# Performance work log

Measured on AMD Instinct MI355X. Metric: run time of the kernel, lower is better.

## Reference

```python
import jax, jax.numpy as jnp
import numpy as np

B = 48        # graphs per batch
NODES = 330   # hardcoded in forward (x.view(batch_size, 330, hidden))
N = B * NODES # 15840 nodes
DEG = 16
E = N * DEG   # 253440 edges
IN_CH = 128
HID = 256
OUT_CH = 1
EDGE_DIM = 5
EPS = 1e-5


def _lin(key, out_f, in_f):
    k1, k2 = jax.random.split(key)
    s = 1.0 / np.sqrt(in_f)
    W = jax.random.uniform(k1, (out_f, in_f), minval=-s, maxval=s, dtype=jnp.float32)
    b = jax.random.uniform(k2, (out_f,), minval=-s, maxval=s, dtype=jnp.float32)
    return W, b


def setup_inputs() -> dict:
    key = jax.random.key(0)
    ks = jax.random.split(key, 10)
    x = jax.random.normal(ks[0], (N, IN_CH), dtype=jnp.float32)
    edge_index = jax.random.randint(ks[1], (2, E), 0, N, dtype=jnp.int32)
    edge_attr = jax.random.normal(ks[2], (E, EDGE_DIM), dtype=jnp.float32)
    batch = (jnp.arange(N, dtype=jnp.int32) // NODES)
    Wq, bq = _lin(ks[3], HID, IN_CH)
    Wk, bk = _lin(ks[4], HID, IN_CH)
    Wv, bv = _lin(ks[5], HID, IN_CH)
    se = 1.0 / np.sqrt(EDGE_DIM)
    We = jax.random.uniform(ks[6], (HID, EDGE_DIM), minval=-se, maxval=se, dtype=jnp.float32)  # lin_edge, bias=False
    Wskip, bskip = _lin(ks[7], HID, IN_CH)
    ln_g = jnp.ones((IN_CH,), jnp.float32); ln_b = jnp.zeros((IN_CH,), jnp.float32)
    bn_g = jnp.ones((HID,), jnp.float32); bn_b = jnp.zeros((HID,), jnp.float32)
    W1, b1 = _lin(ks[8], HID, HID)
    Wr, br = _lin(ks[9], OUT_CH, HID)
    return dict(x=x, edge_index=edge_index, edge_attr=edge_attr, batch=batch,
                Wq=Wq, bq=bq, Wk=Wk, bk=bk, Wv=Wv, bv=bv, We=We,
                Wskip=Wskip, bskip=bskip, ln_g=ln_g, ln_b=ln_b,
                bn_g=bn_g, bn_b=bn_b, W1=W1, b1=b1, Wr=Wr, br=br)


def _forward(x, edge_index, edge_attr, batch,
             Wq, bq, Wk, bk, Wv, bv, We, Wskip, bskip,
             ln_g, ln_b, bn_g, bn_b, W1, b1, Wr, br):
    n = x.shape[0]
    bs = batch.shape[0] // NODES
    # self.norm -> assumed LayerNorm over features
    mu = x.mean(-1, keepdims=True)
    var = x.var(-1, keepdims=True)
    x = (x - mu) / jnp.sqrt(var + EPS) * ln_g + ln_b

    # TransformerConv (heads=1, edge_dim=5, root_weight=True)
    src, dst = edge_index[0], edge_index[1]
    q = x @ Wq.T + bq                      # [N, HID]
    k = x @ Wk.T + bk
    v = x @ Wv.T + bv
    e = edge_attr @ We.T                   # [E, HID]
    ke = k[src] + e                        # edge-conditioned keys
    ve = v[src] + e                        # edge-conditioned values
    alpha = (q[dst] * ke).sum(-1) / jnp.sqrt(jnp.float32(HID))  # [E]
    m = jax.ops.segment_max(alpha, dst, num_segments=n)
    a = jnp.exp(alpha - m[dst])
    z = jax.ops.segment_sum(a, dst, num_segments=n)
    a = a / (z[dst] + 1e-16)               # PyG softmax guard
    out = jax.ops.segment_sum(a[:, None] * ve, dst, num_segments=n)
    out = out + x @ Wskip.T + bskip        # root/skip connection

    # BatchNorm1d (training-mode batch stats) + relu
    bm = out.mean(0)
    bv_ = out.var(0)
    out = (out - bm) / jnp.sqrt(bv_ + EPS) * bn_g + bn_b
    out = jax.nn.relu(out)

    # pooling chain over the node axis: 330 -> 110 -> 36 -> 18
    h = out.reshape(bs, NODES, HID).transpose(0, 2, 1)   # [B, HID, 330]
    h = h.reshape(bs, HID, 110, 3).max(-1)               # k3 s3
    h = h[:, :, :108].reshape(bs, HID, 36, 3).max(-1)    # k3 s3 (floor)
    h = h.reshape(bs, HID, 18, 2).max(-1)                # k2 s2
    h = h.transpose(0, 2, 1)                             # [B, 18, HID]

    h = jax.nn.relu(h @ W1.T + b1)
    c = (h @ Wr.T + br).mean(axis=1)                     # [B, OUT]
    return jax.nn.sigmoid(c).squeeze(-1)                 # [B]


def reference(x, edge_index, edge_attr, batch, Wq, bq, Wk, bk, Wv, bv, We,
              Wskip, bskip, ln_g, ln_b, bn_g, bn_b, W1, b1, Wr, br):
    return _forward(x, edge_index, edge_attr, batch, Wq, bq, Wk, bk, Wv, bv,
                    We, Wskip, bskip, ln_g, ln_b, bn_g, bn_b, W1, b1, Wr, br)
```

## Files before the change

kernel.cpp:

```cpp
#include <hip/hip_runtime.h>
#include <math.h>

#define NNODES 15840
#define NEDGES 253440
#define INCH 128
#define HIDC 256
#define BGR 48
#define GNODES 330

__device__ inline unsigned short f2bf(float f) {
  union { float f; unsigned int u; } v; v.f = f;
  unsigned int u = v.u;
  u += 0x7fff + ((u >> 16) & 1);
  return (unsigned short)(u >> 16);
}
__device__ inline float bf2f(unsigned short h) {
  union { unsigned int u; float f; } v; v.u = ((unsigned int)h) << 16;
  return v.f;
}

__global__ void ln_kernel(const float* __restrict__ x, const float* __restrict__ g,
                          const float* __restrict__ b, float* __restrict__ xln) {
  int wid = (blockIdx.x * blockDim.x + threadIdx.x) >> 6;
  int lane = threadIdx.x & 63;
  if (wid >= NNODES) return;
  float2 v = *(const float2*)(x + (size_t)wid * INCH + lane * 2);
  float s = v.x + v.y;
#pragma unroll
  for (int o = 32; o > 0; o >>= 1) s += __shfl_xor(s, o);
  float mean = s * (1.0f / INCH);
  float d0 = v.x - mean, d1 = v.y - mean;
  float sq = d0 * d0 + d1 * d1;
#pragma unroll
  for (int o = 32; o > 0; o >>= 1) sq += __shfl_xor(sq, o);
  float rstd = rsqrtf(sq * (1.0f / INCH) + 1e-5f);
  float2 gg = *(const float2*)(g + lane * 2);
  float2 bb = *(const float2*)(b + lane * 2);
  float2 o2;
  o2.x = d0 * rstd * gg.x + bb.x;
  o2.y = d1 * rstd * gg.y + bb.y;
  *(float2*)(xln + (size_t)wid * INCH + lane * 2) = o2;
}

#define GBM 128
#define GBN 128
#define GBK 32
#define KD 128
__global__ __launch_bounds__(256) void gemm_qkvs(
    const float* __restrict__ xln,
    const float* __restrict__ Wq, const float* __restrict__ bq,
    const float* __restrict__ Wk, const float* __restrict__ bk,
    const float* __restrict__ Wv, const float* __restrict__ bv,
    const float* __restrict__ Ws, const float* __restrict__ bs,
    float* __restrict__ QS, unsigned short* __restrict__ KV) {
  __shared__ float As[GBK][GBM];
  __shared__ float Bs[GBK][GBN];
  int t = threadIdx.x;
  int m0 = blockIdx.x * GBM;
  int jb = blockIdx.y;
  int mat = jb >> 1;
  const float* W; const float* bias;
  switch (mat) {
    case 0:  W = Wq; bias = bq; break;
    case 1:  W = Wk; bias = bk; break;
    case 2:  W = Wv; bias = bv; break;
    default: W = Ws; bias = bs; break;
  }
  int j0 = (jb & 1) * GBN;

  int r = t & 127;
  int half = t >> 7;
  int tx = t & 15, ty = t >> 4;

  int gr = m0 + r;
  bool okA = gr < NNODES;
  const float* arow = xln + (size_t)gr * KD;
  const float* brow = W + (size_t)(j0 + r) * KD;

  float acc[8][8] = {};

  for (int k0 = 0; k0 < KD; k0 += GBK) {
#pragma unroll
    for (int i = 0; i < 4; i++) {
      int lk = half * 16 + i * 4;
      int kc = k0 + lk;
      float4 av = okA ? *(const float4*)(arow + kc) : make_float4(0.f, 0.f, 0.f, 0.f);
      As[lk + 0][r] = av.x; As[lk + 1][r] = av.y;
      As[lk + 2][r] = av.z; As[lk + 3][r] = av.w;
      float4 bvv = *(const float4*)(brow + kc);
      Bs[lk + 0][r] = bvv.x; Bs[lk + 1][r] = bvv.y;
      Bs[lk + 2][r] = bvv.z; Bs[lk + 3][r] = bvv.w;
    }
    __syncthreads();
#pragma unroll 2
    for (int k = 0; k < GBK; k++) {
      float4 a0 = *(const float4*)&As[k][ty * 4];
      float4 a1 = *(const float4*)&As[k][64 + ty * 4];
      float4 b0 = *(const float4*)&Bs[k][tx * 4];
      float4 b1 = *(const float4*)&Bs[k][64 + tx * 4];
      float aa[8] = {a0.x, a0.y, a0.z, a0.w, a1.x, a1.y, a1.z, a1.w};
      float bb[8] = {b0.x, b0.y, b0.z, b0.w, b1.x, b1.y, b1.z, b1.w};
#pragma unroll
      for (int ar = 0; ar < 8; ar++)
#pragma unroll
        for (int ac = 0; ac < 8; ac++) acc[ar][ac] += aa[ar] * bb[ac];
    }
    __syncthreads();
  }

  float4 bb0 = *(const float4*)(bias + j0 + tx * 4);
  float4 bb1 = *(const float4*)(bias + j0 + 64 + tx * 4);
  int sec = (mat == 0 || mat == 1) ? 0 : 256;
  bool isF32 = (mat == 0 || mat == 3);
  int col0 = sec + j0 + tx * 4;
#pragma unroll
  for (int ar = 0; ar < 8; ar++) {
    int grow = m0 + ((ar < 4) ? (ty * 4 + ar) : (64 + ty * 4 + ar - 4));
    if (grow < NNODES) {
      float4 o0, o1;
      o0.x = acc[ar][0] + bb0.x; o0.y = acc[ar][1] + bb0.y;
      o0.z = acc[ar][2] + bb0.z; o0.w = acc[ar][3] + bb0.w;
      o1.x = acc[ar][4] + bb1.x; o1.y = acc[ar][5] + bb1.y;
      o1.z = acc[ar][6] + bb1.z; o1.w = acc[ar][7] + bb1.w;
      if (isF32) {
        *(float4*)(QS + (size_t)grow * 512 + col0) = o0;
        *(float4*)(QS + (size_t)grow * 512 + col0 + 64) = o1;
      } else {
        ushort4 h0, h1;
        h0.x = f2bf(o0.x); h0.y = f2bf(o0.y); h0.z = f2bf(o0.z); h0.w = f2bf(o0.w);
        h1.x = f2bf(o1.x); h1.y = f2bf(o1.y); h1.z = f2bf(o1.z); h1.w = f2bf(o1.w);
        *(ushort4*)(KV + (size_t)grow * 512 + col0) = h0;
        *(ushort4*)(KV + (size_t)grow * 512 + col0 + 64) = h1;
      }
    }
  }
}

__global__ void count_kernel(const int* __restrict__ dst, int* __restrict__ deg) {
  int e = blockIdx.x * blockDim.x + threadIdx.x;
  if (e < NEDGES) atomicAdd(&deg[dst[e]], 1);
}

__global__ void scan_kernel(const int* __restrict__ deg, int* __restrict__ row_start) {
  __shared__ int wsum[16];
  __shared__ int carry_s;
  int t = threadIdx.x;
  int lane = t & 63, w = t >> 6;
  if (t == 0) carry_s = 0;
  __syncthreads();
  for (int base = 0; base < NNODES; base += 1024) {
    int i = base + t;
    int v = (i < NNODES) ? deg[i] : 0;
    int inc = v;
#pragma unroll
    for (int o = 1; o < 64; o <<= 1) {
      int nv = __shfl_up(inc, o);
      if (lane >= o) inc += nv;
    }
    if (lane == 63) wsum[w] = inc;
    __syncthreads();
    if (w == 0 && lane < 16) {
      int ws = wsum[lane];
#pragma unroll
      for (int o = 1; o < 16; o <<= 1) {
        int nv = __shfl_up(ws, o);
        if (lane >= o) ws += nv;
      }
      wsum[lane] = ws;
    }
    __syncthreads();
    int wexcl = (w > 0) ? wsum[w - 1] : 0;
    int chunk_total = wsum[15];
    int cl = carry_s;
    if (i < NNODES) row_start[i] = cl + wexcl + inc - v;
    __syncthreads();
    if (t == 0) carry_s += chunk_total;
  }
  __syncthreads();
  if (t == 0) row_start[NNODES] = carry_s;
}

__global__ void scatter_kernel(const int* __restrict__ src, const int* __restrict__ dst,
                               const int* __restrict__ row_start, int* __restrict__ cursor,
                               const float* __restrict__ ea, int* __restrict__ src_perm,
                               float* __restrict__ ea_perm) {
  int e = blockIdx.x * blockDim.x + threadIdx.x;
  if (e < NEDGES) {
    int d = dst[e];
    int pos = row_start[d] + atomicAdd(&cursor[d], 1);
    src_perm[pos] = src[e];
    const float* ap = ea + (size_t)e * 5;
    float* op = ea_perm + (size_t)pos * 5;
#pragma unroll
    for (int i = 0; i < 5; i++) op[i] = ap[i];
  }
}

__global__ __launch_bounds__(256) void agg_kernel(
    const float* __restrict__ QS, const unsigned short* __restrict__ KV,
    const float* __restrict__ ea_perm, const float* __restrict__ We,
    const int* __restrict__ src_perm, const int* __restrict__ row_start,
    float* __restrict__ outb) {
  int t = threadIdx.x;
  int nd = blockIdx.x * 4 + (t >> 6);
  int lane = t & 63;
  if (nd >= NNODES) return;

  float4 q = *(const float4*)(QS + (size_t)nd * 512 + 4 * lane);

  float c5[5];
  {
    float wp0[5], wp1[5], wp2[5], wp3[5];
#pragma unroll
    for (int d = 0; d < 5; d++) {
      wp0[d] = We[(4 * lane + 0) * 5 + d];
      wp1[d] = We[(4 * lane + 1) * 5 + d];
      wp2[d] = We[(4 * lane + 2) * 5 + d];
      wp3[d] = We[(4 * lane + 3) * 5 + d];
    }
#pragma unroll
    for (int d = 0; d < 5; d++) {
      float s = q.x * wp0[d] + q.y * wp1[d] + q.z * wp2[d] + q.w * wp3[d];
#pragma unroll
      for (int o = 32; o > 0; o >>= 1) s += __shfl_xor(s, o);
      c5[d] = s;
    }
  }

  int beg = row_start[nd], end = row_start[nd + 1];
  float m = -INFINITY, z = 0.0f;
  float ax = 0.f, ay = 0.f, az = 0.f, aw = 0.f;
  float ea_acc[5] = {0.f, 0.f, 0.f, 0.f, 0.f};

  int j = beg;
  for (; j + 4 <= end; j += 4) {
    int s0 = src_perm[j], s1 = src_perm[j + 1], s2 = src_perm[j + 2], s3 = src_perm[j + 3];
    const unsigned short* b0 = KV + (size_t)s0 * 512 + 4 * lane;
    const unsigned short* b1 = KV + (size_t)s1 * 512 + 4 * lane;
    const unsigned short* b2 = KV + (size_t)s2 * 512 + 4 * lane;
    const unsigned short* b3 = KV + (size_t)s3 * 512 + 4 * lane;
    ushort4 hk0 = *(const ushort4*)b0;
    ushort4 hk1 = *(const ushort4*)b1;
    ushort4 hk2 = *(const ushort4*)b2;
    ushort4 hk3 = *(const ushort4*)b3;
    ushort4 hv0 = *(const ushort4*)(b0 + 256);
    ushort4 hv1 = *(const ushort4*)(b1 + 256);
    ushort4 hv2 = *(const ushort4*)(b2 + 256);
    ushort4 hv3 = *(const ushort4*)(b3 + 256);
    float eat[4][5];
    {
      const float* ap = ea_perm + (size_t)j * 5;
#pragma unroll
      for (int i = 0; i < 4; i++)
#pragma unroll
        for (int d = 0; d < 5; d++) eat[i][d] = ap[i * 5 + d];
    }
    float p0 = q.x * bf2f(hk0.x) + q.y * bf2f(hk0.y) + q.z * bf2f(hk0.z) + q.w * bf2f(hk0.w);
    float p1 = q.x * bf2f(hk1.x) + q.y * bf2f(hk1.y) + q.z * bf2f(hk1.z) + q.w * bf2f(hk1.w);
    float p2 = q.x * bf2f(hk2.x) + q.y * bf2f(hk2.y) + q.z * bf2f(hk2.z) + q.w * bf2f(hk2.w);
    float p3 = q.x * bf2f(hk3.x) + q.y * bf2f(hk3.y) + q.z * bf2f(hk3.z) + q.w * bf2f(hk3.w);
#pragma unroll
    for (int o = 32; o > 0; o >>= 1) {
      p0 += __shfl_xor(p0, o); p1 += __shfl_xor(p1, o);
      p2 += __shfl_xor(p2, o); p3 += __shfl_xor(p3, o);
    }
    float dt0 = 0.f, dt1 = 0.f, dt2 = 0.f, dt3 = 0.f;
#pragma unroll
    for (int d = 0; d < 5; d++) {
      dt0 += c5[d] * eat[0][d]; dt1 += c5[d] * eat[1][d];
      dt2 += c5[d] * eat[2][d]; dt3 += c5[d] * eat[3][d];
    }
    float al0 = (p0 + dt0) * 0.0625f, al1 = (p1 + dt1) * 0.0625f;
    float al2 = (p2 + dt2) * 0.0625f, al3 = (p3 + dt3) * 0.0625f;
    float bm = fmaxf(fmaxf(al0, al1), fmaxf(al2, al3));
    float nm = fmaxf(m, bm);
    float sc = __expf(m - nm);
    float w0 = __expf(al0 - nm), w1 = __expf(al1 - nm);
    float w2 = __expf(al2 - nm), w3 = __expf(al3 - nm);
    z = z * sc + (w0 + w1 + w2 + w3);
    ax = ax * sc + w0 * bf2f(hv0.x) + w1 * bf2f(hv1.x) + w2 * bf2f(hv2.x) + w3 * bf2f(hv3.x);
    ay = ay * sc + w0 * bf2f(hv0.y) + w1 * bf2f(hv1.y) + w2 * bf2f(hv2.y) + w3 * bf2f(hv3.y);
    az = az * sc + w0 * bf2f(hv0.z) + w1 * bf2f(hv1.z) + w2 * bf2f(hv2.z) + w3 * bf2f(hv3.z);
    aw = aw * sc + w0 * bf2f(hv0.w) + w1 * bf2f(hv1.w) + w2 * bf2f(hv2.w) + w3 * bf2f(hv3.w);
#pragma unroll
    for (int d = 0; d < 5; d++)
      ea_acc[d] = ea_acc[d] * sc + w0 * eat[0][d] + w1 * eat[1][d] + w2 * eat[2][d] + w3 * eat[3][d];
    m = nm;
  }
  for (; j < end; j++) {
    int s = src_perm[j];
    const unsigned short* bp = KV + (size_t)s * 512 + 4 * lane;
    ushort4 hk = *(const ushort4*)bp;
    ushort4 hv = *(const ushort4*)(bp + 256);
    float eat[5];
    const float* ap = ea_perm + (size_t)j * 5;
#pragma unroll
    for (int d = 0; d < 5; d++) eat[d] = ap[d];
    float p = q.x * bf2f(hk.x) + q.y * bf2f(hk.y) + q.z * bf2f(hk.z) + q.w * bf2f(hk.w);
#pragma unroll
    for (int o = 32; o > 0; o >>= 1) p += __shfl_xor(p, o);
    float dt = 0.f;
#pragma unroll
    for (int d = 0; d < 5; d++) dt += c5[d] * eat[d];
    float al = (p + dt) * 0.0625f;
    float nm = fmaxf(m, al);
    float sc = __expf(m - nm);
    float w = __expf(al - nm);
    z = z * sc + w;
    ax = ax * sc + w * bf2f(hv.x); ay = ay * sc + w * bf2f(hv.y);
    az = az * sc + w * bf2f(hv.z); aw = aw * sc + w * bf2f(hv.w);
#pragma unroll
    for (int d = 0; d < 5; d++) ea_acc[d] = ea_acc[d] * sc + w * eat[d];
    m = nm;
  }

  float inv = 1.0f / (z + 1e-16f);
  float4 sk = *(const float4*)(QS + (size_t)nd * 512 + 256 + 4 * lane);
  float efx = 0.f, efy = 0.f, efz = 0.f, efw = 0.f;
#pragma unroll
  for (int d = 0; d < 5; d++) {
    float ead = ea_acc[d];
    efx += We[(4 * lane + 0) * 5 + d] * ead;
    efy += We[(4 * lane + 1) * 5 + d] * ead;
    efz += We[(4 * lane + 2) * 5 + d] * ead;
    efw += We[(4 * lane + 3) * 5 + d] * ead;
  }
  float4 o;
  o.x = (ax + efx) * inv + sk.x;
  o.y = (ay + efy) * inv + sk.y;
  o.z = (az + efz) * inv + sk.z;
  o.w = (aw + efw) * inv + sk.w;
  *(float4*)(outb + (size_t)nd * HIDC + 4 * lane) = o;
}

__global__ void bnstat_kernel(const float* __restrict__ outb, float* __restrict__ sums,
                              float* __restrict__ sumsq) {
  int f = threadIdx.x;
  int r0 = blockIdx.x * 120;
  float s = 0.0f, sq = 0.0f;
  for (int r = 0; r < 120; r++) {
    float v = outb[(size_t)(r0 + r) * HIDC + f];
    s += v; sq += v * v;
  }
  atomicAdd(&sums[f], s);
  atomicAdd(&sumsq[f], sq);
}

__global__ void pool_mlp_kernel(const float* __restrict__ outb, const float* __restrict__ sums,
                                const float* __restrict__ sumsq, const float* __restrict__ bng,
                                const float* __restrict__ bnb, const float* __restrict__ W1,
                                const float* __restrict__ b1, const float* __restrict__ Wr,
                                float* __restrict__ c) {
  __shared__ float hs[HIDC];
  __shared__ float red[HIDC];
  int bt = blockIdx.x, t = threadIdx.x;
  int b = bt / 18, tt = bt % 18;
  float mean = sums[t] * (1.0f / NNODES);
  float var = sumsq[t] * (1.0f / NNODES) - mean * mean;
  float scale = bng[t] * rsqrtf(var + 1e-5f);
  float shift = bnb[t] - mean * scale;
  int base = b * GNODES + tt * 18;
  float mx = -INFINITY;
  for (int r = 0; r < 18; r++) {
    float v = outb[(size_t)(base + r) * HIDC + t];
    mx = fmaxf(mx, fmaxf(v * scale + shift, 0.0f));
  }
  hs[t] = mx;
  __syncthreads();
  const float4* hv = (const float4*)hs;
  const float4* w = (const float4*)(W1 + t * HIDC);
  float acc = b1[t];
#pragma unroll 8
  for (int i = 0; i < HIDC / 4; i++) {
    float4 xi = hv[i]; float4 ww = w[i];
    acc += xi.x * ww.x + xi.y * ww.y + xi.z * ww.z + xi.w * ww.w;
  }
  red[t] = fmaxf(acc, 0.0f) * Wr[t];
  __syncthreads();
#pragma unroll
  for (int s = 128; s > 0; s >>= 1) {
    if (t < s) red[t] += red[t + s];
    __syncthreads();
  }
  if (t == 0) atomicAdd(&c[b], red[0] * (1.0f / 18.0f));
}

__global__ void final_kernel(const float* __restrict__ c, const float* __restrict__ br,
                             float* __restrict__ out) {
  int b = threadIdx.x;
  if (b < BGR) out[b] = 1.0f / (1.0f + expf(-(c[b] + br[0])));
}

extern "C" void kernel_launch(void* const* d_in, const int* in_sizes, int n_in,
                              void* d_out, int out_size, void* d_ws, size_t ws_size,
                              hipStream_t stream) {
  const float* x   = (const float*)d_in[0];
  const int*   ei  = (const int*)d_in[1];
  const float* ea  = (const float*)d_in[2];
  const float* Wq  = (const float*)d_in[4];  const float* bq  = (const float*)d_in[5];
  const float* Wk  = (const float*)d_in[6];  const float* bk  = (const float*)d_in[7];
  const float* Wv  = (const float*)d_in[8];  const float* bv  = (const float*)d_in[9];
  const float* We  = (const float*)d_in[10];
  const float* Wsk = (const float*)d_in[11]; const float* bsk = (const float*)d_in[12];
  const float* lng = (const float*)d_in[13]; const float* lnb = (const float*)d_in[14];
  const float* bng = (const float*)d_in[15]; const float* bnb = (const float*)d_in[16];
  const float* W1  = (const float*)d_in[17]; const float* b1  = (const float*)d_in[18];
  const float* Wr  = (const float*)d_in[19]; const float* br  = (const float*)d_in[20];
  float* outp = (float*)d_out;

  const int* srcArr = ei;
  const int* dstArr = ei + NEDGES;

  char* ws = (char*)d_ws;
  size_t off = 0;
  auto alloc = [&](size_t bytes) -> void* {
    void* p = ws + off;
    off += (bytes + 255) & ~(size_t)255;
    return p;
  };
  float*          xln       = (float*)alloc((size_t)NNODES * INCH * 4);
  float*          QS        = (float*)alloc((size_t)NNODES * 512 * 4);
  unsigned short* KV        = (unsigned short*)alloc((size_t)NNODES * 512 * 2);
  float*          outb      = (float*)alloc((size_t)NNODES * HIDC * 4);
  int*            row_start = (int*)alloc((size_t)(NNODES + 1) * 4);
  int*            src_perm  = (int*)alloc((size_t)NEDGES * 4);
  float*          ea_perm   = (float*)alloc((size_t)NEDGES * 5 * 4);
  size_t zn = (size_t)NNODES * 2 + HIDC * 2 + BGR;
  int* zblock = (int*)alloc(zn * 4);
  int*   deg    = zblock;
  int*   cursor = zblock + NNODES;
  float* sums   = (float*)(zblock + 2 * NNODES);
  float* sumsq  = sums + HIDC;
  float* cacc   = sumsq + HIDC;

  hipMemsetAsync(zblock, 0, zn * 4, stream);

  ln_kernel<<<NNODES / 4, 256, 0, stream>>>(x, lng, lnb, xln);
  dim3 ggrid((NNODES + GBM - 1) / GBM, 8);
  gemm_qkvs<<<ggrid, 256, 0, stream>>>(xln, Wq, bq, Wk, bk, Wv, bv, Wsk, bsk, QS, KV);
  count_kernel<<<NEDGES / 256, 256, 0, stream>>>(dstArr, deg);
  scan_kernel<<<1, 1024, 0, stream>>>(deg, row_start);
  scatter_kernel<<<NEDGES / 256, 256, 0, stream>>>(srcArr, dstArr, row_start, cursor, ea,
                                                   src_perm, ea_perm);
  agg_kernel<<<NNODES / 4, 256, 0, stream>>>(QS, KV, ea_perm, We, src_perm, row_start, outb);
  bnstat_kernel<<<132, 256, 0, stream>>>(outb, sums, sumsq);
  pool_mlp_kernel<<<BGR * 18, 256, 0, stream>>>(outb, sums, sumsq, bng, bnb, W1, b1, Wr, cacc);
  final_kernel<<<1, 64, 0, stream>>>(cacc, br, outp);
}
```

Measured before the change: 296.7 us.

## Use split-bf16 MFMA projection GEMM and fixed-slot edge buckets in a fused prep kernel

```diff
diff --git a/kernel.cpp b/kernel.cpp
--- a/kernel.cpp
+++ b/kernel.cpp
@@ -7,6 +7,10 @@
 #define HIDC 256
 #define BGR 48
 #define GNODES 330
+#define SLOT 56
+
+typedef __attribute__((ext_vector_type(8))) short bf16x8;
+typedef __attribute__((ext_vector_type(4))) float f32x4;
 
 __device__ inline unsigned short f2bf(float f) {
   union { float f; unsigned int u; } v; v.f = f;
@@ -19,187 +23,158 @@
   return v.f;
 }
 
-__global__ void ln_kernel(const float* __restrict__ x, const float* __restrict__ g,
-                          const float* __restrict__ b, float* __restrict__ xln) {
-  int wid = (blockIdx.x * blockDim.x + threadIdx.x) >> 6;
-  int lane = threadIdx.x & 63;
-  if (wid >= NNODES) return;
-  float2 v = *(const float2*)(x + (size_t)wid * INCH + lane * 2);
-  float s = v.x + v.y;
-#pragma unroll
-  for (int o = 32; o > 0; o >>= 1) s += __shfl_xor(s, o);
-  float mean = s * (1.0f / INCH);
-  float d0 = v.x - mean, d1 = v.y - mean;
-  float sq = d0 * d0 + d1 * d1;
-#pragma unroll
-  for (int o = 32; o > 0; o >>= 1) sq += __shfl_xor(sq, o);
-  float rstd = rsqrtf(sq * (1.0f / INCH) + 1e-5f);
-  float2 gg = *(const float2*)(g + lane * 2);
-  float2 bb = *(const float2*)(b + lane * 2);
-  float2 o2;
-  o2.x = d0 * rstd * gg.x + bb.x;
-  o2.y = d1 * rstd * gg.y + bb.y;
-  *(float2*)(xln + (size_t)wid * INCH + lane * 2) = o2;
-}
-
-#define GBM 128
-#define GBN 128
-#define GBK 32
-#define KD 128
-__global__ __launch_bounds__(256) void gemm_qkvs(
-    const float* __restrict__ xln,
+#define LN_BLOCKS 3960
+#define WC_BLOCKS 128
+#define BUILD_BLOCKS 990
+__global__ __launch_bounds__(256) void prep_kernel(
+    const float* __restrict__ x, const float* __restrict__ g, const float* __restrict__ b,
+    unsigned short* __restrict__ Xhi, unsigned short* __restrict__ Xlo,
     const float* __restrict__ Wq, const float* __restrict__ bq,
     const float* __restrict__ Wk, const float* __restrict__ bk,
     const float* __restrict__ Wv, const float* __restrict__ bv,
     const float* __restrict__ Ws, const float* __restrict__ bs,
+    unsigned short* __restrict__ Whi, unsigned short* __restrict__ Wlo,
+    float* __restrict__ bbig,
+    const int* __restrict__ src, const int* __restrict__ dst,
+    const float* __restrict__ ea, int* __restrict__ cursor,
+    int* __restrict__ src_perm, float* __restrict__ ea_perm) {
+  int blk = blockIdx.x, t = threadIdx.x;
+  if (blk < LN_BLOCKS) {
+    int wid = blk * 4 + (t >> 6);
+    int lane = t & 63;
+    float2 v = *(const float2*)(x + (size_t)wid * INCH + lane * 2);
+    float s = v.x + v.y;
+#pragma unroll
+    for (int o = 32; o > 0; o >>= 1) s += __shfl_xor(s, o);
+    float mean = s * (1.0f / INCH);
+    float d0 = v.x - mean, d1 = v.y - mean;
+    float sq = d0 * d0 + d1 * d1;
+#pragma unroll
+    for (int o = 32; o > 0; o >>= 1) sq += __shfl_xor(sq, o);
+    float rstd = rsqrtf(sq * (1.0f / INCH) + 1e-5f);
+    float2 gg = *(const float2*)(g + lane * 2);
+    float2 bb = *(const float2*)(b + lane * 2);
+    float o0 = d0 * rstd * gg.x + bb.x;
+    float o1 = d1 * rstd * gg.y + bb.y;
+    unsigned short h0 = f2bf(o0), h1 = f2bf(o1);
+    unsigned short l0 = f2bf(o0 - bf2f(h0)), l1 = f2bf(o1 - bf2f(h1));
+    ushort2 hh; hh.x = h0; hh.y = h1;
+    ushort2 ll; ll.x = l0; ll.y = l1;
+    *(ushort2*)(Xhi + (size_t)wid * INCH + lane * 2) = hh;
+    *(ushort2*)(Xlo + (size_t)wid * INCH + lane * 2) = ll;
+  } else if (blk < LN_BLOCKS + WC_BLOCKS) {
+    int idx = (blk - LN_BLOCKS) * 256 + t;
+    int n = idx >> 5;
+    int k0 = (idx & 31) * 4;
+    const float* W; const float* bias;
+    switch (n >> 8) {
+      case 0:  W = Wq; bias = bq; break;
+      case 1:  W = Wk; bias = bk; break;
+      case 2:  W = Wv; bias = bv; break;
+      default: W = Ws; bias = bs; break;
+    }
+    int r = n & 255;
+    float4 w4 = *(const float4*)(W + (size_t)r * 128 + k0);
+    ushort4 hi, lo;
+    hi.x = f2bf(w4.x); lo.x = f2bf(w4.x - bf2f(hi.x));
+    hi.y = f2bf(w4.y); lo.y = f2bf(w4.y - bf2f(hi.y));
+    hi.z = f2bf(w4.z); lo.z = f2bf(w4.z - bf2f(hi.z));
+    hi.w = f2bf(w4.w); lo.w = f2bf(w4.w - bf2f(hi.w));
+    *(ushort4*)(Whi + (size_t)n * 128 + k0) = hi;
+    *(ushort4*)(Wlo + (size_t)n * 128 + k0) = lo;
+    if (idx < 1024) {
+      const float* bsrc;
+      switch (idx >> 8) {
+        case 0:  bsrc = bq; break;
+        case 1:  bsrc = bk; break;
+        case 2:  bsrc = bv; break;
+        default: bsrc = bs; break;
+      }
+      bbig[idx] = bsrc[idx & 255];
+    }
+  } else {
+    int e = (blk - LN_BLOCKS - WC_BLOCKS) * 256 + t;
+    if (e < NEDGES) {
+      int d = dst[e];
+      int pos = atomicAdd(&cursor[d], 1);
+      if (pos < SLOT) {
+        int slot = d * SLOT + pos;
+        src_perm[slot] = src[e];
+        const float* ap = ea + (size_t)e * 5;
+        float* op = ea_perm + (size_t)slot * 5;
+#pragma unroll
+        for (int i = 0; i < 5; i++) op[i] = ap[i];
+      }
+    }
+  }
+}
+
+__global__ __launch_bounds__(64) void gemm_mfma(
+    const unsigned short* __restrict__ Xhi, const unsigned short* __restrict__ Xlo,
+    const unsigned short* __restrict__ Whi, const unsigned short* __restrict__ Wlo,
+    const float* __restrict__ bbig,
     float* __restrict__ QS, unsigned short* __restrict__ KV) {
-  __shared__ float As[GBK][GBM];
-  __shared__ float Bs[GBK][GBN];
-  int t = threadIdx.x;
-  int m0 = blockIdx.x * GBM;
-  int jb = blockIdx.y;
-  int mat = jb >> 1;
-  const float* W; const float* bias;
-  switch (mat) {
-    case 0:  W = Wq; bias = bq; break;
-    case 1:  W = Wk; bias = bk; break;
-    case 2:  W = Wv; bias = bv; break;
-    default: W = Ws; bias = bs; break;
-  }
-  int j0 = (jb & 1) * GBN;
-
-  int r = t & 127;
-  int half = t >> 7;
-  int tx = t & 15, ty = t >> 4;
-
-  int gr = m0 + r;
-  bool okA = gr < NNODES;
-  const float* arow = xln + (size_t)gr * KD;
-  const float* brow = W + (size_t)(j0 + r) * KD;
-
-  float acc[8][8] = {};
-
-  for (int k0 = 0; k0 < KD; k0 += GBK) {
-#pragma unroll
-    for (int i = 0; i < 4; i++) {
-      int lk = half * 16 + i * 4;
-      int kc = k0 + lk;
-      float4 av = okA ? *(const float4*)(arow + kc) : make_float4(0.f, 0.f, 0.f, 0.f);
-      As[lk + 0][r] = av.x; As[lk + 1][r] = av.y;
-      As[lk + 2][r] = av.z; As[lk + 3][r] = av.w;
-      float4 bvv = *(const float4*)(brow + kc);
-      Bs[lk + 0][r] = bvv.x; Bs[lk + 1][r] = bvv.y;
-      Bs[lk + 2][r] = bvv.z; Bs[lk + 3][r] = bvv.w;
-    }
-    __syncthreads();
-#pragma unroll 2
-    for (int k = 0; k < GBK; k++) {
-      float4 a0 = *(const float4*)&As[k][ty * 4];
-      float4 a1 = *(const float4*)&As[k][64 + ty * 4];
-      float4 b0 = *(const float4*)&Bs[k][tx * 4];
-      float4 b1 = *(const float4*)&Bs[k][64 + tx * 4];
-      float aa[8] = {a0.x, a0.y, a0.z, a0.w, a1.x, a1.y, a1.z, a1.w};
-      float bb[8] = {b0.x, b0.y, b0.z, b0.w, b1.x, b1.y, b1.z, b1.w};
-#pragma unroll
-      for (int ar = 0; ar < 8; ar++)
-#pragma unroll
-        for (int ac = 0; ac < 8; ac++) acc[ar][ac] += aa[ar] * bb[ac];
-    }
-    __syncthreads();
-  }
-
-  float4 bb0 = *(const float4*)(bias + j0 + tx * 4);
-  float4 bb1 = *(const float4*)(bias + j0 + 64 + tx * 4);
-  int sec = (mat == 0 || mat == 1) ? 0 : 256;
-  bool isF32 = (mat == 0 || mat == 3);
-  int col0 = sec + j0 + tx * 4;
-#pragma unroll
-  for (int ar = 0; ar < 8; ar++) {
-    int grow = m0 + ((ar < 4) ? (ty * 4 + ar) : (64 + ty * 4 + ar - 4));
-    if (grow < NNODES) {
-      float4 o0, o1;
-      o0.x = acc[ar][0] + bb0.x; o0.y = acc[ar][1] + bb0.y;
-      o0.z = acc[ar][2] + bb0.z; o0.w = acc[ar][3] + bb0.w;
-      o1.x = acc[ar][4] + bb1.x; o1.y = acc[ar][5] + bb1.y;
-      o1.z = acc[ar][6] + bb1.z; o1.w = acc[ar][7] + bb1.w;
-      if (isF32) {
-        *(float4*)(QS + (size_t)grow * 512 + col0) = o0;
-        *(float4*)(QS + (size_t)grow * 512 + col0 + 64) = o1;
-      } else {
-        ushort4 h0, h1;
-        h0.x = f2bf(o0.x); h0.y = f2bf(o0.y); h0.z = f2bf(o0.z); h0.w = f2bf(o0.w);
-        h1.x = f2bf(o1.x); h1.y = f2bf(o1.y); h1.z = f2bf(o1.z); h1.w = f2bf(o1.w);
-        *(ushort4*)(KV + (size_t)grow * 512 + col0) = h0;
-        *(ushort4*)(KV + (size_t)grow * 512 + col0 + 64) = h1;
+  int lane = threadIdx.x;
+  int m0 = blockIdx.x * 32;
+  int quad = lane >> 4;
+  int lr = lane & 15;
+
+  bf16x8 A[2][2][4];
+#pragma unroll
+  for (int tI = 0; tI < 2; tI++) {
+    const unsigned short* ph = Xhi + (size_t)(m0 + tI * 16 + lr) * 128 + quad * 8;
+    const unsigned short* pl = Xlo + (size_t)(m0 + tI * 16 + lr) * 128 + quad * 8;
+#pragma unroll
+    for (int kf = 0; kf < 4; kf++) {
+      A[tI][0][kf] = *(const bf16x8*)(ph + kf * 32);
+      A[tI][1][kf] = *(const bf16x8*)(pl + kf * 32);
+    }
+  }
+
+  for (int nt = 0; nt < 64; nt++) {
+    int n0 = nt * 16;
+    const unsigned short* wh = Whi + (size_t)(n0 + lr) * 128 + quad * 8;
+    const unsigned short* wl = Wlo + (size_t)(n0 + lr) * 128 + quad * 8;
+    bf16x8 Bh[4], Bl[4];
+#pragma unroll
+    for (int kf = 0; kf < 4; kf++) {
+      Bh[kf] = *(const bf16x8*)(wh + kf * 32);
+      Bl[kf] = *(const bf16x8*)(wl + kf * 32);
+    }
+    f32x4 acc0 = {0.f, 0.f, 0.f, 0.f}, acc1 = {0.f, 0.f, 0.f, 0.f};
+#pragma unroll
+    for (int kf = 0; kf < 4; kf++) {
+      acc0 = __builtin_amdgcn_mfma_f32_16x16x32_bf16(A[0][0][kf], Bh[kf], acc0, 0, 0, 0);
+      acc1 = __builtin_amdgcn_mfma_f32_16x16x32_bf16(A[1][0][kf], Bh[kf], acc1, 0, 0, 0);
+      acc0 = __builtin_amdgcn_mfma_f32_16x16x32_bf16(A[0][0][kf], Bl[kf], acc0, 0, 0, 0);
+      acc1 = __builtin_amdgcn_mfma_f32_16x16x32_bf16(A[1][0][kf], Bl[kf], acc1, 0, 0, 0);
+      acc0 = __builtin_amdgcn_mfma_f32_16x16x32_bf16(A[0][1][kf], Bh[kf], acc0, 0, 0, 0);
+      acc1 = __builtin_amdgcn_mfma_f32_16x16x32_bf16(A[1][1][kf], Bh[kf], acc1, 0, 0, 0);
+    }
+    int col = n0 + lr;
+    float bias = bbig[col];
+    int mat = col >> 8;
+    int cc = col & 255;
+    int base_off = (mat == 0) ? cc : (mat == 3) ? 256 + cc : (mat == 1) ? cc : 256 + cc;
+    bool isF32 = (mat == 0 || mat == 3);
+#pragma unroll
+    for (int tI = 0; tI < 2; tI++) {
+      f32x4 a = tI ? acc1 : acc0;
+#pragma unroll
+      for (int r = 0; r < 4; r++) {
+        int row = m0 + tI * 16 + quad * 4 + r;
+        float val = a[r] + bias;
+        if (isF32) QS[(size_t)row * 512 + base_off] = val;
+        else       KV[(size_t)row * 512 + base_off] = f2bf(val);
       }
     }
-  }
-}
-
-__global__ void count_kernel(const int* __restrict__ dst, int* __restrict__ deg) {
-  int e = blockIdx.x * blockDim.x + threadIdx.x;
-  if (e < NEDGES) atomicAdd(&deg[dst[e]], 1);
-}
-
-__global__ void scan_kernel(const int* __restrict__ deg, int* __restrict__ row_start) {
-  __shared__ int wsum[16];
-  __shared__ int carry_s;
-  int t = threadIdx.x;
-  int lane = t & 63, w = t >> 6;
-  if (t == 0) carry_s = 0;
-  __syncthreads();
-  for (int base = 0; base < NNODES; base += 1024) {
-    int i = base + t;
-    int v = (i < NNODES) ? deg[i] : 0;
-    int inc = v;
-#pragma unroll
-    for (int o = 1; o < 64; o <<= 1) {
-      int nv = __shfl_up(inc, o);
-      if (lane >= o) inc += nv;
-    }
-    if (lane == 63) wsum[w] = inc;
-    __syncthreads();
-    if (w == 0 && lane < 16) {
-      int ws = wsum[lane];
-#pragma unroll
-      for (int o = 1; o < 16; o <<= 1) {
-        int nv = __shfl_up(ws, o);
-        if (lane >= o) ws += nv;
-      }
-      wsum[lane] = ws;
-    }
-    __syncthreads();
-    int wexcl = (w > 0) ? wsum[w - 1] : 0;
-    int chunk_total = wsum[15];
-    int cl = carry_s;
-    if (i < NNODES) row_start[i] = cl + wexcl + inc - v;
-    __syncthreads();
-    if (t == 0) carry_s += chunk_total;
-  }
-  __syncthreads();
-  if (t == 0) row_start[NNODES] = carry_s;
-}
-
-__global__ void scatter_kernel(const int* __restrict__ src, const int* __restrict__ dst,
-                               const int* __restrict__ row_start, int* __restrict__ cursor,
-                               const float* __restrict__ ea, int* __restrict__ src_perm,
-                               float* __restrict__ ea_perm) {
-  int e = blockIdx.x * blockDim.x + threadIdx.x;
-  if (e < NEDGES) {
-    int d = dst[e];
-    int pos = row_start[d] + atomicAdd(&cursor[d], 1);
-    src_perm[pos] = src[e];
-    const float* ap = ea + (size_t)e * 5;
-    float* op = ea_perm + (size_t)pos * 5;
-#pragma unroll
-    for (int i = 0; i < 5; i++) op[i] = ap[i];
   }
 }
 
 __global__ __launch_bounds__(256) void agg_kernel(
     const float* __restrict__ QS, const unsigned short* __restrict__ KV,
     const float* __restrict__ ea_perm, const float* __restrict__ We,
-    const int* __restrict__ src_perm, const int* __restrict__ row_start,
+    const int* __restrict__ src_perm, const int* __restrict__ cursor,
     float* __restrict__ outb) {
   int t = threadIdx.x;
   int nd = blockIdx.x * 4 + (t >> 6);
@@ -227,7 +202,8 @@
     }
   }
 
-  int beg = row_start[nd], end = row_start[nd + 1];
+  int deg = cursor[nd]; if (deg > SLOT) deg = SLOT;
+  int beg = nd * SLOT, end = beg + deg;
   float m = -INFINITY, z = 0.0f;
   float ax = 0.f, ay = 0.f, az = 0.f, aw = 0.f;
   float ea_acc[5] = {0.f, 0.f, 0.f, 0.f, 0.f};
@@ -418,31 +394,30 @@
     off += (bytes + 255) & ~(size_t)255;
     return p;
   };
-  float*          xln       = (float*)alloc((size_t)NNODES * INCH * 4);
-  float*          QS        = (float*)alloc((size_t)NNODES * 512 * 4);
-  unsigned short* KV        = (unsigned short*)alloc((size_t)NNODES * 512 * 2);
-  float*          outb      = (float*)alloc((size_t)NNODES * HIDC * 4);
-  int*            row_start = (int*)alloc((size_t)(NNODES + 1) * 4);
-  int*            src_perm  = (int*)alloc((size_t)NEDGES * 4);
-  float*          ea_perm   = (float*)alloc((size_t)NEDGES * 5 * 4);
-  size_t zn = (size_t)NNODES * 2 + HIDC * 2 + BGR;
+  unsigned short* Xhi      = (unsigned short*)alloc((size_t)NNODES * INCH * 2);
+  unsigned short* Xlo      = (unsigned short*)alloc((size_t)NNODES * INCH * 2);
+  unsigned short* Whi      = (unsigned short*)alloc((size_t)1024 * 128 * 2);
+  unsigned short* Wlo      = (unsigned short*)alloc((size_t)1024 * 128 * 2);
+  float*          bbig     = (float*)alloc(1024 * 4);
+  float*          QS       = (float*)alloc((size_t)NNODES * 512 * 4);
+  unsigned short* KV       = (unsigned short*)alloc((size_t)NNODES * 512 * 2);
+  float*          outb     = (float*)alloc((size_t)NNODES * HIDC * 4);
+  int*            src_perm = (int*)alloc((size_t)NNODES * SLOT * 4);
+  float*          ea_perm  = (float*)alloc((size_t)NNODES * SLOT * 5 * 4);
+  size_t zn = (size_t)NNODES + HIDC * 2 + BGR;
   int* zblock = (int*)alloc(zn * 4);
-  int*   deg    = zblock;
-  int*   cursor = zblock + NNODES;
-  float* sums   = (float*)(zblock + 2 * NNODES);
+  int*   cursor = zblock;
+  float* sums   = (float*)(zblock + NNODES);
   float* sumsq  = sums + HIDC;
   float* cacc   = sumsq + HIDC;
 
   hipMemsetAsync(zblock, 0, zn * 4, stream);
 
-  ln_kernel<<<NNODES / 4, 256, 0, stream>>>(x, lng, lnb, xln);
-  dim3 ggrid((NNODES + GBM - 1) / GBM, 8);
-  gemm_qkvs<<<ggrid, 256, 0, stream>>>(xln, Wq, bq, Wk, bk, Wv, bv, Wsk, bsk, QS, KV);
-  count_kernel<<<NEDGES / 256, 256, 0, stream>>>(dstArr, deg);
-  scan_kernel<<<1, 1024, 0, stream>>>(deg, row_start);
-  scatter_kernel<<<NEDGES / 256, 256, 0, stream>>>(srcArr, dstArr, row_start, cursor, ea,
-                                                   src_perm, ea_perm);
-  agg_kernel<<<NNODES / 4, 256, 0, stream>>>(QS, KV, ea_perm, We, src_perm, row_start, outb);
+  prep_kernel<<<LN_BLOCKS + WC_BLOCKS + BUILD_BLOCKS, 256, 0, stream>>>(
+      x, lng, lnb, Xhi, Xlo, Wq, bq, Wk, bk, Wv, bv, Wsk, bsk, Whi, Wlo, bbig,
+      srcArr, dstArr, ea, cursor, src_perm, ea_perm);
+  gemm_mfma<<<NNODES / 32, 64, 0, stream>>>(Xhi, Xlo, Whi, Wlo, bbig, QS, KV);
+  agg_kernel<<<NNODES / 4, 256, 0, stream>>>(QS, KV, ea_perm, We, src_perm, cursor, outb);
   bnstat_kernel<<<132, 256, 0, stream>>>(outb, sums, sumsq);
   pool_mlp_kernel<<<BGR * 18, 256, 0, stream>>>(outb, sums, sumsq, bng, bnb, W1, b1, Wr, cacc);
   final_kernel<<<1, 64, 0, stream>>>(cacc, br, outp);
```

Result: slower. 309.9 us (+4.5%).
